# Performance work log

Measured on AMD Instinct MI355X. Metric: run time of the kernel, lower is better.

## Reference

```python
import jax, jax.numpy as jnp
import numpy as np

TAU = 0.1          # tau_default
K = 4              # temporal_low_freq_k
EPS = 1e-06        # charbonnier_eps


def _lowpass_proj(T: int, k: int) -> jnp.ndarray:
    """P = D_k^T @ D_k where D_k are the first k rows of the orthonormal DCT-II
    matrix. x @ P == idct(dct(x, norm='ortho') * mask_k, norm='ortho') along last axis."""
    t = jnp.arange(T, dtype=jnp.float32)
    n = jnp.arange(k, dtype=jnp.float32)
    D = jnp.sqrt(2.0 / T) * jnp.cos(jnp.pi * (2.0 * t[None, :] + 1.0) * n[:, None] / (2.0 * T))
    D = D.at[0].multiply(1.0 / jnp.sqrt(2.0))  # ortho scaling of DC row
    return D.T @ D  # [T, T], rank k


def setup_inputs() -> dict:
    key = jax.random.key(0)
    k1, k2 = jax.random.split(key)
    shape = (4, 16, 32, 128, 128)  # [B, C, T, H, W]
    x_star_T = jax.random.normal(k1, shape, dtype=jnp.float32)
    x_target_T = jax.random.normal(k2, shape, dtype=jnp.float32)
    return {"x_star_T": x_star_T, "x_target_T": x_target_T}


def reference(x_star_T, x_target_T):
    x_star = x_star_T.astype(jnp.float32)
    x_tgt = x_target_T.astype(jnp.float32)

    # Charbonnier main loss
    diff = x_star - x_tgt
    L_main = jnp.mean(jnp.sqrt(diff * diff + EPS * EPS))

    # Temporal low-pass (DCT -> keep first K -> IDCT) as a single [T,T] matmul
    T = x_star.shape[2]
    P = _lowpass_proj(T, K)
    x_star_low = jnp.einsum('bcthw,ts->bcshw', x_star, P)
    x_tgt_low = jnp.einsum('bcthw,ts->bcshw', x_tgt, P)

    # Temporal diff MSE
    d_pred = x_star_low[:, :, 1:] - x_star_low[:, :, :-1]
    d_gt = x_tgt_low[:, :, 1:] - x_tgt_low[:, :, :-1]
    L_temp = jnp.mean((d_pred - d_gt) ** 2)

    total = L_main + TAU * L_temp
    return (total, L_main, L_temp)
```

## Files before the change

### kernel.cpp

```cpp
#include <hip/hip_runtime.h>
#include <math.h>

#define B_  4
#define C_  16
#define T_  32
#define H_  128
#define W_  128
#define KF  4
#define TAU 0.1
#define EPS2 (1e-6f * 1e-6f)

#define HW4   ((H_ * W_) / 4)
#define NCOLS (B_ * C_ * HW4)
#define N_MAIN ((double)B_ * C_ * T_ * H_ * W_)
#define N_TEMP ((double)B_ * C_ * (T_ - 1) * H_ * W_)

struct Consts {
    float D[KF][T_];
    float M[KF][KF];
};

__global__ __launch_bounds__(256)
void loss_main_kernel(const float4* __restrict__ xs,
                      const float4* __restrict__ xt,
                      double* __restrict__ acc,
                      Consts con)
{
    const int p  = blockIdx.x * 256 + threadIdx.x;
    const int bc = p >> 12;
    const int hw = p & 4095;
    const size_t base = (size_t)bc * (T_ * HW4) + hw;
    const float4* A  = xs + base;
    const float4* Bp = xt + base;

    float charb = 0.f;
    float c[KF][4];
    #pragma unroll
    for (int n = 0; n < KF; ++n)
        #pragma unroll
        for (int j = 0; j < 4; ++j) c[n][j] = 0.f;

    #pragma unroll
    for (int t = 0; t < T_; ++t) {
        float4 a = A[(size_t)t * HW4];
        float4 b = Bp[(size_t)t * HW4];
        float d[4];
        d[0] = a.x - b.x; d[1] = a.y - b.y; d[2] = a.z - b.z; d[3] = a.w - b.w;
        #pragma unroll
        for (int j = 0; j < 4; ++j)
            charb += sqrtf(fmaf(d[j], d[j], EPS2));
        #pragma unroll
        for (int n = 0; n < KF; ++n) {
            const float w = con.D[n][t];
            #pragma unroll
            for (int j = 0; j < 4; ++j)
                c[n][j] = fmaf(w, d[j], c[n][j]);
        }
    }

    float quad = 0.f;
    #pragma unroll
    for (int j = 0; j < 4; ++j) {
        #pragma unroll
        for (int n = 1; n < KF; ++n) {
            float e = 0.f;
            #pragma unroll
            for (int m = 1; m < KF; ++m)
                e = fmaf(con.M[n][m], c[m][j], e);
            quad = fmaf(c[n][j], e, quad);
        }
    }

    #pragma unroll
    for (int off = 32; off > 0; off >>= 1) {
        charb += __shfl_down(charb, off, 64);
        quad  += __shfl_down(quad,  off, 64);
    }

    __shared__ float s_ch[4], s_q[4];
    const int lane = threadIdx.x & 63;
    const int wave = threadIdx.x >> 6;
    if (lane == 0) { s_ch[wave] = charb; s_q[wave] = quad; }
    __syncthreads();

    if (threadIdx.x == 0) {
        double ch = (double)s_ch[0] + (double)s_ch[1] + (double)s_ch[2] + (double)s_ch[3];
        double q  = (double)s_q[0]  + (double)s_q[1]  + (double)s_q[2]  + (double)s_q[3];
        atomicAdd(&acc[0], ch);
        atomicAdd(&acc[1], q);
    }
}

__global__ void loss_final_kernel(const double* __restrict__ acc,
                                  float* __restrict__ out)
{
    if (threadIdx.x == 0) {
        double Lm = acc[0] / N_MAIN;
        double Lt = acc[1] / N_TEMP;
        out[0] = (float)(Lm + TAU * Lt);
        out[1] = (float)Lm;
        out[2] = (float)Lt;
    }
}

extern "C" void kernel_launch(void* const* d_in, const int* in_sizes, int n_in,
                              void* d_out, int out_size, void* d_ws, size_t ws_size,
                              hipStream_t stream)
{
    const float4* xs = (const float4*)d_in[0];
    const float4* xt = (const float4*)d_in[1];
    float* out = (float*)d_out;
    double* acc = (double*)d_ws;

    Consts con;
    for (int n = 0; n < KF; ++n) {
        for (int t = 0; t < T_; ++t) {
            double v = sqrt(2.0 / (double)T_) *
                       cos(M_PI * (2.0 * t + 1.0) * n / (2.0 * T_));
            if (n == 0) v *= 1.0 / sqrt(2.0);
            con.D[n][t] = (float)v;
        }
    }
    for (int n = 0; n < KF; ++n) {
        for (int m = 0; m < KF; ++m) {
            double s = 0.0;
            for (int ss = 0; ss < T_ - 1; ++ss) {
                double en = (double)con.D[n][ss + 1] - (double)con.D[n][ss];
                double em = (double)con.D[m][ss + 1] - (double)con.D[m][ss];
                s += en * em;
            }
            con.M[n][m] = (float)s;
        }
    }

    hipMemsetAsync(d_ws, 0, 2 * sizeof(double), stream);

    loss_main_kernel<<<NCOLS / 256, 256, 0, stream>>>(xs, xt, acc, con);
    loss_final_kernel<<<1, 64, 0, stream>>>(acc, out);
}
```

Measured before the change: 282.8 us.

## Split temporal axis across two thread halves and batch loads per step

```diff
diff --git a/kernel.cpp b/kernel.cpp
--- a/kernel.cpp
+++ b/kernel.cpp
@@ -12,6 +12,7 @@
 
 #define HW4   ((H_ * W_) / 4)
 #define NCOLS (B_ * C_ * HW4)
+#define CPB   128
 #define N_MAIN ((double)B_ * C_ * T_ * H_ * W_)
 #define N_TEMP ((double)B_ * C_ * (T_ - 1) * H_ * W_)
 
@@ -26,48 +27,76 @@
                       double* __restrict__ acc,
                       Consts con)
 {
-    const int p  = blockIdx.x * 256 + threadIdx.x;
-    const int bc = p >> 12;
-    const int hw = p & 4095;
+    const int col  = threadIdx.x & (CPB - 1);
+    const int half = threadIdx.x >> 7;
+    const int p    = blockIdx.x * CPB + col;
+    const int bc   = p >> 12;
+    const int hw   = p & 4095;
     const size_t base = (size_t)bc * (T_ * HW4) + hw;
     const float4* A  = xs + base;
     const float4* Bp = xt + base;
+    const int t0 = half * (T_ / 2);
 
     float charb = 0.f;
-    float c[KF][4];
+    float c[KF - 1][4];
     #pragma unroll
-    for (int n = 0; n < KF; ++n)
+    for (int n = 0; n < KF - 1; ++n)
         #pragma unroll
         for (int j = 0; j < 4; ++j) c[n][j] = 0.f;
 
     #pragma unroll
-    for (int t = 0; t < T_; ++t) {
-        float4 a = A[(size_t)t * HW4];
-        float4 b = Bp[(size_t)t * HW4];
-        float d[4];
-        d[0] = a.x - b.x; d[1] = a.y - b.y; d[2] = a.z - b.z; d[3] = a.w - b.w;
+    for (int tb = 0; tb < T_ / 2; tb += 4) {
+        float4 a[4], b[4];
         #pragma unroll
-        for (int j = 0; j < 4; ++j)
-            charb += sqrtf(fmaf(d[j], d[j], EPS2));
+        for (int u = 0; u < 4; ++u) {
+            a[u] = A[(size_t)(t0 + tb + u) * HW4];
+            b[u] = Bp[(size_t)(t0 + tb + u) * HW4];
+        }
         #pragma unroll
-        for (int n = 0; n < KF; ++n) {
-            const float w = con.D[n][t];
+        for (int u = 0; u < 4; ++u) {
+            const int t = t0 + tb + u;
+            float d[4];
+            d[0] = a[u].x - b[u].x; d[1] = a[u].y - b[u].y;
+            d[2] = a[u].z - b[u].z; d[3] = a[u].w - b[u].w;
             #pragma unroll
             for (int j = 0; j < 4; ++j)
-                c[n][j] = fmaf(w, d[j], c[n][j]);
+                charb += sqrtf(fmaf(d[j], d[j], EPS2));
+            #pragma unroll
+            for (int n = 0; n < KF - 1; ++n) {
+                const float w = con.D[n + 1][t];
+                #pragma unroll
+                for (int j = 0; j < 4; ++j)
+                    c[n][j] = fmaf(w, d[j], c[n][j]);
+            }
         }
     }
 
+    __shared__ float s_c[(KF - 1) * 4][CPB];
     float quad = 0.f;
-    #pragma unroll
-    for (int j = 0; j < 4; ++j) {
+    if (half == 1) {
         #pragma unroll
-        for (int n = 1; n < KF; ++n) {
-            float e = 0.f;
+        for (int n = 0; n < KF - 1; ++n)
             #pragma unroll
-            for (int m = 1; m < KF; ++m)
-                e = fmaf(con.M[n][m], c[m][j], e);
-            quad = fmaf(c[n][j], e, quad);
+            for (int j = 0; j < 4; ++j)
+                s_c[n * 4 + j][col] = c[n][j];
+    }
+    __syncthreads();
+    if (half == 0) {
+        #pragma unroll
+        for (int n = 0; n < KF - 1; ++n)
+            #pragma unroll
+            for (int j = 0; j < 4; ++j)
+                c[n][j] += s_c[n * 4 + j][col];
+        #pragma unroll
+        for (int j = 0; j < 4; ++j) {
+            #pragma unroll
+            for (int n = 0; n < KF - 1; ++n) {
+                float e = 0.f;
+                #pragma unroll
+                for (int m = 0; m < KF - 1; ++m)
+                    e = fmaf(con.M[n + 1][m + 1], c[m][j], e);
+                quad = fmaf(c[n][j], e, quad);
+            }
         }
     }
 
@@ -135,6 +164,6 @@
 
     hipMemsetAsync(d_ws, 0, 2 * sizeof(double), stream);
 
-    loss_main_kernel<<<NCOLS / 256, 256, 0, stream>>>(xs, xt, acc, con);
+    loss_main_kernel<<<NCOLS / CPB, 256, 0, stream>>>(xs, xt, acc, con);
     loss_final_kernel<<<1, 64, 0, stream>>>(acc, out);
 }
```

Result: no change. 283.4 us (+0.2%).

## Split time axis across waves with register prefetch and LDS coefficient reduction

Applied to the files above, without the earlier changes.

```diff
diff --git a/kernel.cpp b/kernel.cpp
--- a/kernel.cpp
+++ b/kernel.cpp
@@ -12,62 +12,113 @@
 
 #define HW4   ((H_ * W_) / 4)
 #define NCOLS (B_ * C_ * HW4)
+#define CPB   256
 #define N_MAIN ((double)B_ * C_ * T_ * H_ * W_)
 #define N_TEMP ((double)B_ * C_ * (T_ - 1) * H_ * W_)
+
+typedef float f4 __attribute__((ext_vector_type(4)));
 
 struct Consts {
     float D[KF][T_];
     float M[KF][KF];
 };
 
+__device__ inline f4 fmaf4(float w, f4 d, f4 c) {
+    c.x = fmaf(w, d.x, c.x); c.y = fmaf(w, d.y, c.y);
+    c.z = fmaf(w, d.z, c.z); c.w = fmaf(w, d.w, c.w);
+    return c;
+}
+
 __global__ __launch_bounds__(256)
-void loss_main_kernel(const float4* __restrict__ xs,
-                      const float4* __restrict__ xt,
+void loss_main_kernel(const f4* __restrict__ xs,
+                      const f4* __restrict__ xt,
                       double* __restrict__ acc,
                       Consts con)
 {
-    const int p  = blockIdx.x * 256 + threadIdx.x;
-    const int bc = p >> 12;
-    const int hw = p & 4095;
-    const size_t base = (size_t)bc * (T_ * HW4) + hw;
-    const float4* A  = xs + base;
-    const float4* Bp = xt + base;
+    const int lane = threadIdx.x & 63;
+    const int wave = threadIdx.x >> 6;
+    const int colbase = blockIdx.x * CPB;
+    const int bc = colbase >> 12;
+    const int hw = (colbase & 4095) + lane;
+    const f4* A  = xs + (size_t)bc * (T_ * HW4) + hw;
+    const f4* Bp = xt + (size_t)bc * (T_ * HW4) + hw;
+    const int t0 = wave * (T_ / 4);
 
     float charb = 0.f;
-    float c[KF][4];
+    f4 c[3][4];
     #pragma unroll
-    for (int n = 0; n < KF; ++n)
+    for (int n = 0; n < 3; ++n)
         #pragma unroll
-        for (int j = 0; j < 4; ++j) c[n][j] = 0.f;
+        for (int j = 0; j < 4; ++j) c[n][j] = (f4)(0.f);
+
+    f4 a[4], b[4], a2[4], b2[4];
+    #pragma unroll
+    for (int j = 0; j < 4; ++j) {
+        a[j] = __builtin_nontemporal_load(A  + (size_t)t0 * HW4 + 64 * j);
+        b[j] = __builtin_nontemporal_load(Bp + (size_t)t0 * HW4 + 64 * j);
+    }
 
     #pragma unroll
-    for (int t = 0; t < T_; ++t) {
-        float4 a = A[(size_t)t * HW4];
-        float4 b = Bp[(size_t)t * HW4];
-        float d[4];
-        d[0] = a.x - b.x; d[1] = a.y - b.y; d[2] = a.z - b.z; d[3] = a.w - b.w;
+    for (int tt = 0; tt < T_ / 4; ++tt) {
+        if (tt < T_ / 4 - 1) {
+            #pragma unroll
+            for (int j = 0; j < 4; ++j) {
+                a2[j] = __builtin_nontemporal_load(A  + (size_t)(t0 + tt + 1) * HW4 + 64 * j);
+                b2[j] = __builtin_nontemporal_load(Bp + (size_t)(t0 + tt + 1) * HW4 + 64 * j);
+            }
+        }
+        const int t = t0 + tt;
+        const float w1 = con.D[1][t], w2 = con.D[2][t], w3 = con.D[3][t];
         #pragma unroll
-        for (int j = 0; j < 4; ++j)
-            charb += sqrtf(fmaf(d[j], d[j], EPS2));
-        #pragma unroll
-        for (int n = 0; n < KF; ++n) {
-            const float w = con.D[n][t];
+        for (int j = 0; j < 4; ++j) {
+            f4 d = a[j] - b[j];
+            charb += sqrtf(fmaf(d.x, d.x, EPS2)) + sqrtf(fmaf(d.y, d.y, EPS2))
+                   + sqrtf(fmaf(d.z, d.z, EPS2)) + sqrtf(fmaf(d.w, d.w, EPS2));
+            c[0][j] = fmaf4(w1, d, c[0][j]);
+            c[1][j] = fmaf4(w2, d, c[1][j]);
+            c[2][j] = fmaf4(w3, d, c[2][j]);
+        }
+        if (tt < T_ / 4 - 1) {
             #pragma unroll
-            for (int j = 0; j < 4; ++j)
-                c[n][j] = fmaf(w, d[j], c[n][j]);
+            for (int j = 0; j < 4; ++j) { a[j] = a2[j]; b[j] = b2[j]; }
         }
     }
 
+    __shared__ f4 s_c[3][12][64];
+    if (wave != 0) {
+        #pragma unroll
+        for (int n = 0; n < 3; ++n)
+            #pragma unroll
+            for (int j = 0; j < 4; ++j)
+                s_c[wave - 1][n * 4 + j][lane] = c[n][j];
+    }
+    __syncthreads();
+
     float quad = 0.f;
-    #pragma unroll
-    for (int j = 0; j < 4; ++j) {
+    if (wave == 0) {
         #pragma unroll
-        for (int n = 1; n < KF; ++n) {
-            float e = 0.f;
+        for (int n = 0; n < 3; ++n)
             #pragma unroll
-            for (int m = 1; m < KF; ++m)
-                e = fmaf(con.M[n][m], c[m][j], e);
-            quad = fmaf(c[n][j], e, quad);
+            for (int j = 0; j < 4; ++j) {
+                f4 v = c[n][j];
+                #pragma unroll
+                for (int s = 0; s < 3; ++s)
+                    v += s_c[s][n * 4 + j][lane];
+                c[n][j] = v;
+            }
+        #pragma unroll
+        for (int j = 0; j < 4; ++j) {
+            #pragma unroll
+            for (int n = 0; n < 3; ++n) {
+                f4 e = (f4)(0.f);
+                #pragma unroll
+                for (int m = 0; m < 3; ++m)
+                    e = fmaf4(con.M[n + 1][m + 1], c[m][j], e);
+                quad = fmaf(c[n][j].x, e.x, quad);
+                quad = fmaf(c[n][j].y, e.y, quad);
+                quad = fmaf(c[n][j].z, e.z, quad);
+                quad = fmaf(c[n][j].w, e.w, quad);
+            }
         }
     }
 
@@ -78,8 +129,6 @@
     }
 
     __shared__ float s_ch[4], s_q[4];
-    const int lane = threadIdx.x & 63;
-    const int wave = threadIdx.x >> 6;
     if (lane == 0) { s_ch[wave] = charb; s_q[wave] = quad; }
     __syncthreads();
 
@@ -107,8 +156,8 @@
                               void* d_out, int out_size, void* d_ws, size_t ws_size,
                               hipStream_t stream)
 {
-    const float4* xs = (const float4*)d_in[0];
-    const float4* xt = (const float4*)d_in[1];
+    const f4* xs = (const f4*)d_in[0];
+    const f4* xt = (const f4*)d_in[1];
     float* out = (float*)d_out;
     double* acc = (double*)d_ws;
 
@@ -133,8 +182,8 @@
         }
     }
 
-    hipMemsetAsync(d_ws, 0, 2 * sizeof(double), stream);
+    (void)hipMemsetAsync(d_ws, 0, 2 * sizeof(double), stream);
 
-    loss_main_kernel<<<NCOLS / 256, 256, 0, stream>>>(xs, xt, acc, con);
+    loss_main_kernel<<<NCOLS / CPB, 256, 0, stream>>>(xs, xt, acc, con);
     loss_final_kernel<<<1, 64, 0, stream>>>(acc, out);
 }
```

Result: faster. 265.7 us (-6.1%).
